# Optimization experiments

Measured on AMD Instinct MI355X. Metric: run time of the kernel, lower is better.

## Reference

```python
import jax, jax.numpy as jnp
import numpy as np

B, I, P, T = 128, 64, 16, 5
N_TYPE, VOCAB, D = 3, 100000, 64


def setup_inputs() -> dict:
    key = jax.random.key(0)
    k1, k2, k3, k4, k5 = jax.random.split(key, 5)
    path_input = jax.random.randint(k1, (B, I, P, T), 0, VOCAB, dtype=jnp.int32)
    path_type = jax.random.randint(k2, (T,), 0, N_TYPE, dtype=jnp.int32)
    tables = jax.random.normal(k3, (N_TYPE, VOCAB, D), dtype=jnp.float32) * 0.02
    # nn.Conv1d(D, D, 2): weight [out=D, in=D, k=2], bias [D]
    bound = 1.0 / np.sqrt(D * 2)
    conv_w = jax.random.uniform(k4, (D, D, 2), minval=-bound, maxval=bound, dtype=jnp.float32)
    conv_b = jax.random.uniform(k5, (D,), minval=-bound, maxval=bound, dtype=jnp.float32)
    return {"path_input": path_input, "path_type": path_type,
            "tables": tables, "conv_w": conv_w, "conv_b": conv_b}


def reference(path_input, path_type, tables, conv_w, conv_b):
    b, i, p, t = path_input.shape
    n = b * i
    d = tables.shape[-1]
    vocab = tables.shape[1]
    x = path_input.reshape(n, p, t)
    # per-timestep dynamic-table gather, fused via flat indexing:
    # element (n,p,j) looks up row x[n,p,j] of table path_type[j]
    flat_idx = path_type[None, None, :].astype(jnp.int32) * vocab + x  # [n,p,t]
    emb = tables.reshape(-1, d)[flat_idx]                              # [n,p,t,d]
    # Conv1d kernel_size=2 over the time axis (valid): windows of 2
    xw = jnp.stack([emb[:, :, :-1, :], emb[:, :, 1:, :]], axis=-1)     # [n,p,t-1,d,2]
    y = jnp.einsum('nptik,oik->npto', xw, conv_w) + conv_b             # [n,p,t-1,d]
    # max-pool over remaining time positions (NOTE: no ReLU in original forward)
    pooled = jnp.max(y, axis=2)                                        # [n,p,d]
    # faithful replication of torch.cat(outputs,-1).view(p, n, d) memory trick
    out = pooled.reshape(n, p * d).reshape(p, n, d)                    # [p,n,d]
    out = jnp.max(jnp.transpose(out, (1, 2, 0)), axis=-1)              # [n,d]
    return out.reshape(b, i, d)
```

## Files before the change

### kernel.cpp

```cpp
#include <hip/hip_runtime.h>
#include <hip/hip_bf16.h>

#define B_  128
#define I_  64
#define P_  16
#define T_  5
#define NT  3
#define VOCAB 100000
#define D_  64
#define NPAIR (B_ * I_)
#define OUTROWS NPAIR

__device__ __forceinline__ unsigned short f2b(float f) {
    unsigned int u = __float_as_uint(f);
    return (unsigned short)((u + 0x7fffu + ((u >> 16) & 1u)) >> 16);
}

typedef short short8 __attribute__((ext_vector_type(8)));
typedef float f32x4 __attribute__((ext_vector_type(4)));

#define AROW_STRIDE 160
#define AWAVE_BYTES (80 * AROW_STRIDE)

__global__ __launch_bounds__(256) void wprep(
        const float* __restrict__ convw, unsigned short* __restrict__ Wf) {
    const int e0 = threadIdx.x * 4;
#pragma unroll
    for (int e = e0; e < e0 + 4; ++e) {
        int m = e & 15;
        int quad = (e >> 4) & 3;
        int half = (e >> 6) & 1;
        int cb = e >> 7;
        int c = cb * 16 + m;
        const float* wp = (c < 64) ? (convw + c * 128) : (convw + (c - 64) * 128 + 1);
#pragma unroll
        for (int j = 0; j < 8; ++j) {
            int k = half * 32 + quad * 8 + j;
            Wf[e * 8 + j] = f2b(wp[k * 2]);
        }
    }
}

__global__ __launch_bounds__(256) void fused_path(
        const int* __restrict__ path_input, const int* __restrict__ path_type,
        const float* __restrict__ tables, const unsigned short* __restrict__ Wf,
        const float* __restrict__ bias, float* __restrict__ out) {
    __shared__ __align__(16) unsigned char Asmem[4][AWAVE_BYTES];
    const int tid = threadIdx.x;
    const int w = tid >> 6;
    const int lane = tid & 63;
    const int l16 = lane & 15;
    const int quad = lane >> 4;
    const int r2 = lane >> 4;
    const int c16 = lane & 15;

    const int nn = blockIdx.x * 4 + w;
    const int g = nn >> 4, q = nn & 15;
    unsigned char* myA = Asmem[w];

    short8 WB0[8], WB1[8];
#pragma unroll
    for (int ns = 0; ns < 8; ++ns) {
        WB0[ns] = *(const short8*)&Wf[((ns * 8 + 0 + quad) * 16 + l16) * 8];
        WB1[ns] = *(const short8*)&Wf[((ns * 8 + 4 + quad) * 16 + l16) * 8];
    }

    int roff[20];
#pragma unroll
    for (int i = 0; i < 20; ++i) {
        int t = i >> 2, sub = i & 3;
        int pp = sub * 4 + r2;
        int addr = ((pp * 512 + g) * 16 + q) * 5 + t;
        roff[i] = (path_type[t] * VOCAB + path_input[addr]) * 64;
    }

    float4 F[20];
#pragma unroll
    for (int i = 0; i < 20; ++i)
        F[i] = *(const float4*)(tables + (size_t)roff[i] + c16 * 4);

#pragma unroll
    for (int i = 0; i < 20; ++i) {
        int t = i >> 2, sub = i & 3;
        int R = t * 16 + sub * 4 + r2;
        unsigned int p0 = (unsigned int)f2b(F[i].x) | ((unsigned int)f2b(F[i].y) << 16);
        unsigned int p1 = (unsigned int)f2b(F[i].z) | ((unsigned int)f2b(F[i].w) << 16);
        uint2 pk; pk.x = p0; pk.y = p1;
        *(uint2*)(myA + R * AROW_STRIDE + c16 * 8) = pk;
    }

    short8 A0[5], A1[5];
#pragma unroll
    for (int t = 0; t < 5; ++t) {
        const unsigned char* rp = myA + (t * 16 + l16) * AROW_STRIDE;
        A0[t] = *(const short8*)(rp + quad * 16);
        A1[t] = *(const short8*)(rp + 64 + quad * 16);
    }

    f32x4 runmax[4];
#pragma unroll
    for (int ns = 0; ns < 4; ++ns) runmax[ns] = (f32x4){-1e30f, -1e30f, -1e30f, -1e30f};
#pragma unroll
    for (int to = 0; to < 4; ++to) {
#pragma unroll
        for (int ns = 0; ns < 4; ++ns) {
            f32x4 uu = {0.f, 0.f, 0.f, 0.f};
            uu = __builtin_amdgcn_mfma_f32_16x16x32_bf16(WB0[ns], A0[to], uu, 0, 0, 0);
            uu = __builtin_amdgcn_mfma_f32_16x16x32_bf16(WB1[ns], A1[to], uu, 0, 0, 0);
            f32x4 vv = {0.f, 0.f, 0.f, 0.f};
            vv = __builtin_amdgcn_mfma_f32_16x16x32_bf16(WB0[ns + 4], A0[to + 1], vv, 0, 0, 0);
            vv = __builtin_amdgcn_mfma_f32_16x16x32_bf16(WB1[ns + 4], A1[to + 1], vv, 0, 0, 0);
#pragma unroll
            for (int j = 0; j < 4; ++j)
                runmax[ns][j] = fmaxf(runmax[ns][j], uu[j] + vv[j]);
        }
    }

#pragma unroll
    for (int ns = 0; ns < 4; ++ns) {
#pragma unroll
        for (int j = 0; j < 4; ++j) {
            float v = runmax[ns][j];
            v = fmaxf(v, __shfl_xor(v, 1));
            v = fmaxf(v, __shfl_xor(v, 2));
            v = fmaxf(v, __shfl_xor(v, 4));
            v = fmaxf(v, __shfl_xor(v, 8));
            runmax[ns][j] = v;
        }
    }
    if (l16 == 0) {
#pragma unroll
        for (int ns = 0; ns < 4; ++ns) {
            int c = ns * 16 + quad * 4;
            float4 bv = *(const float4*)(bias + c);
            float4 o;
            o.x = runmax[ns][0] + bv.x;
            o.y = runmax[ns][1] + bv.y;
            o.z = runmax[ns][2] + bv.z;
            o.w = runmax[ns][3] + bv.w;
            *(float4*)(out + (size_t)nn * 64 + c) = o;
        }
    }
}

__global__ __launch_bounds__(64) void fused_direct(
        const int* __restrict__ path_input, const int* __restrict__ path_type,
        const float* __restrict__ tables, const float* __restrict__ convw,
        const float* __restrict__ bias, float* __restrict__ out) {
    const int nn = blockIdx.x;
    const int o = threadIdx.x;
    const int g = nn >> 4;
    const int q = nn & 15;
    float w0[64], w1[64];
#pragma unroll
    for (int i = 0; i < 64; ++i) {
        w0[i] = convw[o * 128 + i * 2];
        w1[i] = convw[o * 128 + i * 2 + 1];
    }
    int tb[5];
#pragma unroll
    for (int t = 0; t < 5; ++t) tb[t] = path_type[t] * VOCAB;
    __shared__ float emb[5][64];
    float acc = -1e30f;
    for (int pp = 0; pp < 16; ++pp) {
        int m = pp * 512 + g;
        const int* ip = path_input + ((m * 16 + q) * 5);
        __syncthreads();
#pragma unroll
        for (int t = 0; t < 5; ++t)
            emb[t][o] = tables[(size_t)(tb[t] + ip[t]) * 64 + o];
        __syncthreads();
#pragma unroll
        for (int to = 0; to < 4; ++to) {
            float s = 0.f;
#pragma unroll
            for (int i = 0; i < 64; ++i)
                s += w0[i] * emb[to][i] + w1[i] * emb[to + 1][i];
            acc = fmaxf(acc, s);
        }
    }
    out[(size_t)nn * 64 + o] = acc + bias[o];
}

extern "C" void kernel_launch(void* const* d_in, const int* in_sizes, int n_in,
                              void* d_out, int out_size, void* d_ws, size_t ws_size,
                              hipStream_t stream) {
    const int*   path_input = (const int*)d_in[0];
    const int*   path_type  = (const int*)d_in[1];
    const float* tables     = (const float*)d_in[2];
    const float* convw      = (const float*)d_in[3];
    const float* convb      = (const float*)d_in[4];
    float* out = (float*)d_out;

    const size_t needWf = (size_t)16 * 1024 * sizeof(unsigned short);
    if (ws_size >= needWf) {
        unsigned short* Wf = (unsigned short*)d_ws;
        wprep<<<1, 256, 0, stream>>>(convw, Wf);
        fused_path<<<OUTROWS / 4, 256, 0, stream>>>(path_input, path_type,
                                                    tables, Wf, convb, out);
    } else {
        fused_direct<<<OUTROWS, 64, 0, stream>>>(path_input, path_type, tables, convw, convb, out);
    }
}
```

Baseline: 132.3 us.

## Fuse weight bf16 prep into main kernel and use hardware pack conversion

Removes the separate weight-prep kernel launch and its workspace round trip. Each wave now loads fp32 conv weights directly and converts them to bf16 MFMA fragments in registers after issuing the embedding gathers. Software bf16 rounding is replaced with the v_cvt_pk_bf16_f32 instruction, and a sched barrier plus launch bounds of 3 blocks per CU are added. The cost is redundant per-wave weight loading and conversion instead of a one-time prep.

```diff
diff --git a/kernel.cpp b/kernel.cpp
--- a/kernel.cpp
+++ b/kernel.cpp
@@ -1,5 +1,4 @@
 #include <hip/hip_runtime.h>
-#include <hip/hip_bf16.h>
 
 #define B_  128
 #define I_  64
@@ -11,39 +10,24 @@
 #define NPAIR (B_ * I_)
 #define OUTROWS NPAIR
 
-__device__ __forceinline__ unsigned short f2b(float f) {
-    unsigned int u = __float_as_uint(f);
-    return (unsigned short)((u + 0x7fffu + ((u >> 16) & 1u)) >> 16);
-}
-
 typedef short short8 __attribute__((ext_vector_type(8)));
 typedef float f32x4 __attribute__((ext_vector_type(4)));
+typedef unsigned int uint4v __attribute__((ext_vector_type(4)));
 
 #define AROW_STRIDE 160
 #define AWAVE_BYTES (80 * AROW_STRIDE)
 
-__global__ __launch_bounds__(256) void wprep(
-        const float* __restrict__ convw, unsigned short* __restrict__ Wf) {
-    const int e0 = threadIdx.x * 4;
-#pragma unroll
-    for (int e = e0; e < e0 + 4; ++e) {
-        int m = e & 15;
-        int quad = (e >> 4) & 3;
-        int half = (e >> 6) & 1;
-        int cb = e >> 7;
-        int c = cb * 16 + m;
-        const float* wp = (c < 64) ? (convw + c * 128) : (convw + (c - 64) * 128 + 1);
-#pragma unroll
-        for (int j = 0; j < 8; ++j) {
-            int k = half * 32 + quad * 8 + j;
-            Wf[e * 8 + j] = f2b(wp[k * 2]);
-        }
-    }
+__device__ __forceinline__ unsigned int cvtpk_bf16(float lo, float hi) {
+    unsigned int r;
+    asm("v_cvt_pk_bf16_f32 %0, %1, %2" : "=v"(r) : "v"(lo), "v"(hi));
+    return r;
 }
 
-__global__ __launch_bounds__(256) void fused_path(
+union S8U { short8 s; uint4v u; };
+
+__global__ __launch_bounds__(256, 3) void fused_one(
         const int* __restrict__ path_input, const int* __restrict__ path_type,
-        const float* __restrict__ tables, const unsigned short* __restrict__ Wf,
+        const float* __restrict__ tables, const float* __restrict__ convw,
         const float* __restrict__ bias, float* __restrict__ out) {
     __shared__ __align__(16) unsigned char Asmem[4][AWAVE_BYTES];
     const int tid = threadIdx.x;
@@ -57,13 +41,6 @@
     const int nn = blockIdx.x * 4 + w;
     const int g = nn >> 4, q = nn & 15;
     unsigned char* myA = Asmem[w];
-
-    short8 WB0[8], WB1[8];
-#pragma unroll
-    for (int ns = 0; ns < 8; ++ns) {
-        WB0[ns] = *(const short8*)&Wf[((ns * 8 + 0 + quad) * 16 + l16) * 8];
-        WB1[ns] = *(const short8*)&Wf[((ns * 8 + 4 + quad) * 16 + l16) * 8];
-    }
 
     int roff[20];
 #pragma unroll
@@ -83,10 +60,39 @@
     for (int i = 0; i < 20; ++i) {
         int t = i >> 2, sub = i & 3;
         int R = t * 16 + sub * 4 + r2;
-        unsigned int p0 = (unsigned int)f2b(F[i].x) | ((unsigned int)f2b(F[i].y) << 16);
-        unsigned int p1 = (unsigned int)f2b(F[i].z) | ((unsigned int)f2b(F[i].w) << 16);
-        uint2 pk; pk.x = p0; pk.y = p1;
+        uint2 pk;
+        pk.x = cvtpk_bf16(F[i].x, F[i].y);
+        pk.y = cvtpk_bf16(F[i].z, F[i].w);
         *(uint2*)(myA + R * AROW_STRIDE + c16 * 8) = pk;
+    }
+
+    __builtin_amdgcn_sched_barrier(0);
+
+    short8 WB0[8], WB1[8];
+#pragma unroll
+    for (int ns = 0; ns < 4; ++ns) {
+        const float* rp = convw + (ns * 16 + l16) * 128 + quad * 16;
+        float4 a0 = *(const float4*)(rp + 0);
+        float4 a1 = *(const float4*)(rp + 4);
+        float4 a2 = *(const float4*)(rp + 8);
+        float4 a3 = *(const float4*)(rp + 12);
+        float4 b0 = *(const float4*)(rp + 64);
+        float4 b1 = *(const float4*)(rp + 68);
+        float4 b2 = *(const float4*)(rp + 72);
+        float4 b3 = *(const float4*)(rp + 76);
+        S8U e, o;
+        e.u = (uint4v){cvtpk_bf16(a0.x, a0.z), cvtpk_bf16(a1.x, a1.z),
+                       cvtpk_bf16(a2.x, a2.z), cvtpk_bf16(a3.x, a3.z)};
+        o.u = (uint4v){cvtpk_bf16(a0.y, a0.w), cvtpk_bf16(a1.y, a1.w),
+                       cvtpk_bf16(a2.y, a2.w), cvtpk_bf16(a3.y, a3.w)};
+        WB0[ns]     = e.s;
+        WB0[ns + 4] = o.s;
+        e.u = (uint4v){cvtpk_bf16(b0.x, b0.z), cvtpk_bf16(b1.x, b1.z),
+                       cvtpk_bf16(b2.x, b2.z), cvtpk_bf16(b3.x, b3.z)};
+        o.u = (uint4v){cvtpk_bf16(b0.y, b0.w), cvtpk_bf16(b1.y, b1.w),
+                       cvtpk_bf16(b2.y, b2.w), cvtpk_bf16(b3.y, b3.w)};
+        WB1[ns]     = e.s;
+        WB1[ns + 4] = o.s;
     }
 
     short8 A0[5], A1[5];
@@ -143,45 +149,6 @@
     }
 }
 
-__global__ __launch_bounds__(64) void fused_direct(
-        const int* __restrict__ path_input, const int* __restrict__ path_type,
-        const float* __restrict__ tables, const float* __restrict__ convw,
-        const float* __restrict__ bias, float* __restrict__ out) {
-    const int nn = blockIdx.x;
-    const int o = threadIdx.x;
-    const int g = nn >> 4;
-    const int q = nn & 15;
-    float w0[64], w1[64];
-#pragma unroll
-    for (int i = 0; i < 64; ++i) {
-        w0[i] = convw[o * 128 + i * 2];
-        w1[i] = convw[o * 128 + i * 2 + 1];
-    }
-    int tb[5];
-#pragma unroll
-    for (int t = 0; t < 5; ++t) tb[t] = path_type[t] * VOCAB;
-    __shared__ float emb[5][64];
-    float acc = -1e30f;
-    for (int pp = 0; pp < 16; ++pp) {
-        int m = pp * 512 + g;
-        const int* ip = path_input + ((m * 16 + q) * 5);
-        __syncthreads();
-#pragma unroll
-        for (int t = 0; t < 5; ++t)
-            emb[t][o] = tables[(size_t)(tb[t] + ip[t]) * 64 + o];
-        __syncthreads();
-#pragma unroll
-        for (int to = 0; to < 4; ++to) {
-            float s = 0.f;
-#pragma unroll
-            for (int i = 0; i < 64; ++i)
-                s += w0[i] * emb[to][i] + w1[i] * emb[to + 1][i];
-            acc = fmaxf(acc, s);
-        }
-    }
-    out[(size_t)nn * 64 + o] = acc + bias[o];
-}
-
 extern "C" void kernel_launch(void* const* d_in, const int* in_sizes, int n_in,
                               void* d_out, int out_size, void* d_ws, size_t ws_size,
                               hipStream_t stream) {
@@ -191,14 +158,8 @@
     const float* convw      = (const float*)d_in[3];
     const float* convb      = (const float*)d_in[4];
     float* out = (float*)d_out;
+    (void)d_ws; (void)ws_size;
 
-    const size_t needWf = (size_t)16 * 1024 * sizeof(unsigned short);
-    if (ws_size >= needWf) {
-        unsigned short* Wf = (unsigned short*)d_ws;
-        wprep<<<1, 256, 0, stream>>>(convw, Wf);
-        fused_path<<<OUTROWS / 4, 256, 0, stream>>>(path_input, path_type,
-                                                    tables, Wf, convb, out);
-    } else {
-        fused_direct<<<OUTROWS, 64, 0, stream>>>(path_input, path_type, tables, convw, convb, out);
-    }
+    fused_one<<<OUTROWS / 4, 256, 0, stream>>>(path_input, path_type,
+                                               tables, convw, convb, out);
 }
```

Result: slower. 153.5 us (+16.0%).

## Swizzle LDS layout, stream weights per output slice, cap registers for occupancy

Applied to the files above, without the earlier changes.

The padded LDS row stride becomes an unpadded 128-byte stride, and an XOR swizzle on the row index avoids bank conflicts while cutting shared memory per block. Weight fragments are no longer preloaded into 16 short8 registers up front. Each output-channel slice now loads its four fragments just before its MFMA loop, with the loop order swapped to keep only one running max live. Launch bounds ask for 4 blocks per CU, which lowers VGPR pressure to raise occupancy for this gather-latency-bound kernel, at the cost of weight loads moving into the compute phase.

```diff
diff --git a/kernel.cpp b/kernel.cpp
--- a/kernel.cpp
+++ b/kernel.cpp
@@ -1,5 +1,4 @@
 #include <hip/hip_runtime.h>
-#include <hip/hip_bf16.h>
 
 #define B_  128
 #define I_  64
@@ -19,7 +18,7 @@
 typedef short short8 __attribute__((ext_vector_type(8)));
 typedef float f32x4 __attribute__((ext_vector_type(4)));
 
-#define AROW_STRIDE 160
+#define AROW_STRIDE 128
 #define AWAVE_BYTES (80 * AROW_STRIDE)
 
 __global__ __launch_bounds__(256) void wprep(
@@ -41,7 +40,7 @@
     }
 }
 
-__global__ __launch_bounds__(256) void fused_path(
+__global__ __launch_bounds__(256, 4) void fused_path(
         const int* __restrict__ path_input, const int* __restrict__ path_type,
         const float* __restrict__ tables, const unsigned short* __restrict__ Wf,
         const float* __restrict__ bias, float* __restrict__ out) {
@@ -58,13 +57,6 @@
     const int g = nn >> 4, q = nn & 15;
     unsigned char* myA = Asmem[w];
 
-    short8 WB0[8], WB1[8];
-#pragma unroll
-    for (int ns = 0; ns < 8; ++ns) {
-        WB0[ns] = *(const short8*)&Wf[((ns * 8 + 0 + quad) * 16 + l16) * 8];
-        WB1[ns] = *(const short8*)&Wf[((ns * 8 + 4 + quad) * 16 + l16) * 8];
-    }
-
     int roff[20];
 #pragma unroll
     for (int i = 0; i < 20; ++i) {
@@ -86,34 +78,40 @@
         unsigned int p0 = (unsigned int)f2b(F[i].x) | ((unsigned int)f2b(F[i].y) << 16);
         unsigned int p1 = (unsigned int)f2b(F[i].z) | ((unsigned int)f2b(F[i].w) << 16);
         uint2 pk; pk.x = p0; pk.y = p1;
-        *(uint2*)(myA + R * AROW_STRIDE + c16 * 8) = pk;
+        int off = (c16 * 8) ^ ((R & 7) << 4);
+        *(uint2*)(myA + R * AROW_STRIDE + off) = pk;
     }
 
     short8 A0[5], A1[5];
 #pragma unroll
     for (int t = 0; t < 5; ++t) {
         const unsigned char* rp = myA + (t * 16 + l16) * AROW_STRIDE;
-        A0[t] = *(const short8*)(rp + quad * 16);
-        A1[t] = *(const short8*)(rp + 64 + quad * 16);
+        int sw = (l16 & 7) << 4;
+        A0[t] = *(const short8*)(rp + ((quad * 16) ^ sw));
+        A1[t] = *(const short8*)(rp + ((64 + quad * 16) ^ sw));
     }
 
     f32x4 runmax[4];
 #pragma unroll
-    for (int ns = 0; ns < 4; ++ns) runmax[ns] = (f32x4){-1e30f, -1e30f, -1e30f, -1e30f};
-#pragma unroll
-    for (int to = 0; to < 4; ++to) {
-#pragma unroll
-        for (int ns = 0; ns < 4; ++ns) {
+    for (int ns = 0; ns < 4; ++ns) {
+        short8 W0lo = *(const short8*)&Wf[((ns * 8 + 0 + quad) * 16 + l16) * 8];
+        short8 W0hi = *(const short8*)&Wf[((ns * 8 + 4 + quad) * 16 + l16) * 8];
+        short8 W1lo = *(const short8*)&Wf[(((ns + 4) * 8 + 0 + quad) * 16 + l16) * 8];
+        short8 W1hi = *(const short8*)&Wf[(((ns + 4) * 8 + 4 + quad) * 16 + l16) * 8];
+        f32x4 rm = {-1e30f, -1e30f, -1e30f, -1e30f};
+#pragma unroll
+        for (int to = 0; to < 4; ++to) {
             f32x4 uu = {0.f, 0.f, 0.f, 0.f};
-            uu = __builtin_amdgcn_mfma_f32_16x16x32_bf16(WB0[ns], A0[to], uu, 0, 0, 0);
-            uu = __builtin_amdgcn_mfma_f32_16x16x32_bf16(WB1[ns], A1[to], uu, 0, 0, 0);
+            uu = __builtin_amdgcn_mfma_f32_16x16x32_bf16(W0lo, A0[to], uu, 0, 0, 0);
+            uu = __builtin_amdgcn_mfma_f32_16x16x32_bf16(W0hi, A1[to], uu, 0, 0, 0);
             f32x4 vv = {0.f, 0.f, 0.f, 0.f};
-            vv = __builtin_amdgcn_mfma_f32_16x16x32_bf16(WB0[ns + 4], A0[to + 1], vv, 0, 0, 0);
-            vv = __builtin_amdgcn_mfma_f32_16x16x32_bf16(WB1[ns + 4], A1[to + 1], vv, 0, 0, 0);
+            vv = __builtin_amdgcn_mfma_f32_16x16x32_bf16(W1lo, A0[to + 1], vv, 0, 0, 0);
+            vv = __builtin_amdgcn_mfma_f32_16x16x32_bf16(W1hi, A1[to + 1], vv, 0, 0, 0);
 #pragma unroll
             for (int j = 0; j < 4; ++j)
-                runmax[ns][j] = fmaxf(runmax[ns][j], uu[j] + vv[j]);
-        }
+                rm[j] = fmaxf(rm[j], uu[j] + vv[j]);
+        }
+        runmax[ns] = rm;
     }
 
 #pragma unroll
```

After: 141.3 us. +6.8%, slower.
